# Optimization experiments

Measured on AMD Instinct MI355X. Metric: run time of the kernel, lower is better.

Reference implementation:

```python
import jax, jax.numpy as jnp
import numpy as np

NOISE_STD = 0.1

def setup_inputs() -> dict:
    key = jax.random.key(0)
    k1, k2, k3, k4 = jax.random.split(key, 4)
    B, S, D, E, NS = 4, 4096, 2048, 64, 10
    x = jax.random.normal(k1, (B, S, D), dtype=jnp.float32)
    W = jax.random.normal(k2, (E, D), dtype=jnp.float32) * (1.0 / np.sqrt(D))
    scale_condition = jax.random.normal(k3, (NS, 1, 1), dtype=jnp.float32)
    noise = jax.random.normal(k4, (B, S, E), dtype=jnp.float32)
    return {"x": x, "W": W, "scale_condition": scale_condition, "noise": noise, "scale_idx": 3}

def reference(x, W, scale_condition, noise, scale_idx):
    TOP_K = 2
    E = W.shape[0]
    # scale modulation: scale_condition[scale_idx] has shape [1,1], broadcasts over [B,S,D]
    scale_factor = scale_condition[scale_idx]
    router_input = x * (1.0 + scale_factor * 0.1)
    # small GEMM: [B,S,D] x [D,E] -> [B,S,E]
    router_logits = jnp.einsum('bsd,ed->bse', router_input, W)
    router_logits = router_logits + noise * NOISE_STD
    routing_probs = jax.nn.softmax(router_logits, axis=-1)
    routing_weights, selected_experts = jax.lax.top_k(routing_probs, TOP_K)
    routing_weights = routing_weights / jnp.sum(routing_weights, axis=-1, keepdims=True)
    # scatter top-k normalized weights into dense [B,S,E] dispatch tensor
    dispatch_tensor = jnp.sum(
        jax.nn.one_hot(selected_experts, E, dtype=routing_weights.dtype)
        * routing_weights[..., None],
        axis=-2,
    )
    return dispatch_tensor, routing_probs, selected_experts
```

## Files before the change

### kernel.cpp

```cpp
#include <hip/hip_runtime.h>
#include <math.h>

#define D        2048
#define E        64
#define NROWS    16384

#define ROWS_PB  32
#define BKC      64
#define NCH      (D / BKC)
#define LDX      72
#define LDW      72
#define BUF_SHORTS 13824
#define WCVT_BYTES ((size_t)2 * E * D * sizeof(unsigned short))

#define LSCALE   2048.0f
#define S1       4.8828125e-4f
#define S2       2.384185791015625e-7f

typedef __attribute__((ext_vector_type(8))) _Float16 f16x8;
typedef __attribute__((ext_vector_type(4))) float f32x4;

__device__ __forceinline__ unsigned short f2h(float f) {
    union { _Float16 h; unsigned short u; } c;
    c.h = (_Float16)f;
    return c.u;
}
__device__ __forceinline__ float h2f(unsigned short u) {
    union { _Float16 h; unsigned short u; } c;
    c.u = u;
    return (float)c.h;
}

__global__ __launch_bounds__(256)
void w_cvt(const float* __restrict__ W,
           unsigned short* __restrict__ whi,
           unsigned short* __restrict__ wlo)
{
    const int i = (blockIdx.x * 256 + threadIdx.x) << 3;
    const float4 a = *(const float4*)(W + i);
    const float4 b = *(const float4*)(W + i + 4);
    float vv[8] = {a.x, a.y, a.z, a.w, b.x, b.y, b.z, b.w};
    unsigned int hw[4], lw[4];
#pragma unroll
    for (int j = 0; j < 4; ++j) {
        const unsigned short h0 = f2h(vv[2*j]);
        const unsigned short h1 = f2h(vv[2*j+1]);
        const unsigned short l0 = f2h((vv[2*j]   - h2f(h0)) * LSCALE);
        const unsigned short l1 = f2h((vv[2*j+1] - h2f(h1)) * LSCALE);
        hw[j] = (unsigned int)h0 | ((unsigned int)h1 << 16);
        lw[j] = (unsigned int)l0 | ((unsigned int)l1 << 16);
    }
    *(uint4*)(whi + i) = make_uint4(hw[0], hw[1], hw[2], hw[3]);
    *(uint4*)(wlo + i) = make_uint4(lw[0], lw[1], lw[2], lw[3]);
}

__global__ __launch_bounds__(256)
void moe_fused(const float* __restrict__ x,
               const unsigned short* __restrict__ whi,
               const unsigned short* __restrict__ wlo,
               const float* __restrict__ scond,
               const int* __restrict__ sidx,
               const float* __restrict__ noise,
               float* __restrict__ dispatch,
               float* __restrict__ probs,
               float* __restrict__ sel)
{
    __shared__ unsigned short smem[2 * BUF_SHORTS];

    const int t = threadIdx.x;
    const int l = t & 63;
    const int w = t >> 6;

    const float factor = 1.0f + 0.1f * scond[sidx[0]];

    const int xrow = t >> 3;
    const int xoct = t & 7;
    const int we_  = t >> 2;
    const int wko  = (t & 3) << 4;

    const int R  = (w >> 1) << 4;
    const int CB = (w & 1) << 5;
    const int fr = l & 15;
    const int fq = l >> 4;

    const int rowG0 = blockIdx.x * ROWS_PB;

    const float* xg = x + (size_t)(rowG0 + xrow) * D + (xoct << 3);
    const unsigned short* wgh = whi + (size_t)we_ * D + wko;
    const unsigned short* wgl = wlo + (size_t)we_ * D + wko;

    f32x4 acc0h = {0.f,0.f,0.f,0.f}, acc0m = {0.f,0.f,0.f,0.f}, acc0l = {0.f,0.f,0.f,0.f};
    f32x4 acc1h = {0.f,0.f,0.f,0.f}, acc1m = {0.f,0.f,0.f,0.f}, acc1l = {0.f,0.f,0.f,0.f};

    float4 xa = *(const float4*)(xg);
    float4 xb = *(const float4*)(xg + 4);
    uint4  wa = *(const uint4*)(wgh);
    uint4  wb = *(const uint4*)(wgh + 8);
    uint4  wc = *(const uint4*)(wgl);
    uint4  wd = *(const uint4*)(wgl + 8);

    for (int c = 0; c < NCH; ++c) {
        unsigned short* base = smem + (c & 1) * BUF_SHORTS;
        unsigned short* xh = base;
        unsigned short* xl = base + 2304;
        unsigned short* wh = base + 4608;
        unsigned short* wl = base + 9216;

        {
            float vv[8] = {xa.x * factor, xa.y * factor, xa.z * factor, xa.w * factor,
                           xb.x * factor, xb.y * factor, xb.z * factor, xb.w * factor};
            unsigned int xhw[4], xlw[4];
#pragma unroll
            for (int j = 0; j < 4; ++j) {
                const unsigned short h0 = f2h(vv[2*j]);
                const unsigned short h1 = f2h(vv[2*j+1]);
                const unsigned short l0 = f2h((vv[2*j]   - h2f(h0)) * LSCALE);
                const unsigned short l1 = f2h((vv[2*j+1] - h2f(h1)) * LSCALE);
                xhw[j] = (unsigned int)h0 | ((unsigned int)h1 << 16);
                xlw[j] = (unsigned int)l0 | ((unsigned int)l1 << 16);
            }
            const int o = xrow * LDX + (xoct << 3);
            *(uint4*)&xh[o] = make_uint4(xhw[0], xhw[1], xhw[2], xhw[3]);
            *(uint4*)&xl[o] = make_uint4(xlw[0], xlw[1], xlw[2], xlw[3]);
        }
        {
            const int o = we_ * LDW + wko;
            *(uint4*)&wh[o]     = wa;
            *(uint4*)&wh[o + 8] = wb;
            *(uint4*)&wl[o]     = wc;
            *(uint4*)&wl[o + 8] = wd;
        }

        __syncthreads();

        if (c + 1 < NCH) {
            const int k0 = (c + 1) << 6;
            xa = *(const float4*)(xg + k0);
            xb = *(const float4*)(xg + k0 + 4);
            wa = *(const uint4*)(wgh + k0);
            wb = *(const uint4*)(wgh + k0 + 8);
            wc = *(const uint4*)(wgl + k0);
            wd = *(const uint4*)(wgl + k0 + 8);
        }

#pragma unroll
        for (int ks = 0; ks < 2; ++ks) {
            const int ko = (ks << 5) + (fq << 3);
            const f16x8 ah  = *(const f16x8*)&xh[(R + fr) * LDX + ko];
            const f16x8 al  = *(const f16x8*)&xl[(R + fr) * LDX + ko];
            const f16x8 b0h = *(const f16x8*)&wh[(CB + fr) * LDW + ko];
            const f16x8 b0l = *(const f16x8*)&wl[(CB + fr) * LDW + ko];
            const f16x8 b1h = *(const f16x8*)&wh[(CB + 16 + fr) * LDW + ko];
            const f16x8 b1l = *(const f16x8*)&wl[(CB + 16 + fr) * LDW + ko];
            acc0h = __builtin_amdgcn_mfma_f32_16x16x32_f16(ah, b0h, acc0h, 0, 0, 0);
            acc0m = __builtin_amdgcn_mfma_f32_16x16x32_f16(ah, b0l, acc0m, 0, 0, 0);
            acc0m = __builtin_amdgcn_mfma_f32_16x16x32_f16(al, b0h, acc0m, 0, 0, 0);
            acc0l = __builtin_amdgcn_mfma_f32_16x16x32_f16(al, b0l, acc0l, 0, 0, 0);
            acc1h = __builtin_amdgcn_mfma_f32_16x16x32_f16(ah, b1h, acc1h, 0, 0, 0);
            acc1m = __builtin_amdgcn_mfma_f32_16x16x32_f16(ah, b1l, acc1m, 0, 0, 0);
            acc1m = __builtin_amdgcn_mfma_f32_16x16x32_f16(al, b1h, acc1m, 0, 0, 0);
            acc1l = __builtin_amdgcn_mfma_f32_16x16x32_f16(al, b1l, acc1l, 0, 0, 0);
        }
    }

    __syncthreads();
    float* lg = (float*)smem;
#pragma unroll
    for (int j = 0; j < 4; ++j) {
        const int rr = R + (fq << 2) + j;
        lg[rr * 68 + CB + fr]      = acc0h[j] + S1 * acc0m[j] + S2 * acc0l[j];
        lg[rr * 68 + CB + 16 + fr] = acc1h[j] + S1 * acc1m[j] + S2 * acc1l[j];
    }
    __syncthreads();

    const int r0 = w << 3;
    float nz[8];
#pragma unroll
    for (int i = 0; i < 8; ++i)
        nz[i] = noise[(size_t)(rowG0 + r0 + i) * E + l];

#pragma unroll 2
    for (int i = 0; i < 8; ++i) {
        const int G = rowG0 + r0 + i;
        const float v = lg[(r0 + i) * 68 + l] + 0.1f * nz[i];

        float m = v;
#pragma unroll
        for (int off = 32; off > 0; off >>= 1)
            m = fmaxf(m, __shfl_xor(m, off, 64));
        const float p = expf(v - m);
        float s = p;
#pragma unroll
        for (int off = 32; off > 0; off >>= 1)
            s += __shfl_xor(s, off, 64);
        const float prob = p / s;
        probs[(size_t)G * E + l] = prob;

        float bv = prob; int bi = l;
#pragma unroll
        for (int off = 32; off > 0; off >>= 1) {
            const float ov = __shfl_xor(bv, off, 64);
            const int   oi = __shfl_xor(bi, off, 64);
            if (ov > bv || (ov == bv && oi < bi)) { bv = ov; bi = oi; }
        }
        float cv = (l == bi) ? -INFINITY : prob;
        int ci = l;
#pragma unroll
        for (int off = 32; off > 0; off >>= 1) {
            const float ov = __shfl_xor(cv, off, 64);
            const int   oi = __shfl_xor(ci, off, 64);
            if (ov > cv || (ov == cv && oi < ci)) { cv = ov; ci = oi; }
        }

        const float sum2 = bv + cv;
        float dval = 0.f;
        if (l == bi) dval = bv / sum2;
        if (l == ci) dval = cv / sum2;
        dispatch[(size_t)G * E + l] = dval;

        if (l == 0) {
            float2 sv; sv.x = (float)bi; sv.y = (float)ci;
            *(float2*)(sel + (size_t)G * 2) = sv;
        }
    }
}

__global__ __launch_bounds__(256)
void gemm_r2(const float* __restrict__ x, const float* __restrict__ W,
             const float* __restrict__ scond, const float* __restrict__ noise,
             const int* __restrict__ sidx, float* __restrict__ logits_out)
{
    __shared__ float4 xsb[32][17];
    __shared__ float4 wsh[64][16];
    const int tid = threadIdx.x;
    const int rowBase = blockIdx.x * 32;
    const float factor = 1.0f + 0.1f * scond[sidx[0]];
    const int xk = tid & 15, xr = tid >> 4, we = tid & 63, wk = tid >> 6;
    const int eg = tid & 15, rg = tid >> 4, e0 = eg << 2;
    float acc[2][4];
#pragma unroll
    for (int i = 0; i < 2; ++i)
#pragma unroll
        for (int j = 0; j < 4; ++j) acc[i][j] = 0.f;
    const float* xg = x + (size_t)rowBase * D;
    float4 xb[2], wb[4];
#pragma unroll
    for (int i = 0; i < 2; ++i)
        xb[i] = *(const float4*)(xg + (xr + 16 * i) * D + (xk << 2));
#pragma unroll
    for (int j = 0; j < 4; ++j)
        wb[j] = *(const float4*)(W + we * D + (wk << 4) + (j << 2));
    for (int t = 0; t < 32; ++t) {
#pragma unroll
        for (int i = 0; i < 2; ++i) {
            float4 v = xb[i];
            v.x *= factor; v.y *= factor; v.z *= factor; v.w *= factor;
            xsb[xr + 16 * i][xk] = v;
        }
        float* wsf = (float*)wsh;
#pragma unroll
        for (int j = 0; j < 4; ++j) {
            const int kk = (wk << 4) + (j << 2);
            wsf[(kk + 0) * E + we] = wb[j].x;
            wsf[(kk + 1) * E + we] = wb[j].y;
            wsf[(kk + 2) * E + we] = wb[j].z;
            wsf[(kk + 3) * E + we] = wb[j].w;
        }
        __syncthreads();
        if (t + 1 < 32) {
            const int k0 = (t + 1) * 64;
#pragma unroll
            for (int i = 0; i < 2; ++i)
                xb[i] = *(const float4*)(xg + (xr + 16 * i) * D + k0 + (xk << 2));
#pragma unroll
            for (int j = 0; j < 4; ++j)
                wb[j] = *(const float4*)(W + we * D + k0 + (wk << 4) + (j << 2));
        }
#pragma unroll
        for (int kg = 0; kg < 16; ++kg) {
            float4 xv[2], wv[4];
#pragma unroll
            for (int i = 0; i < 2; ++i) xv[i] = xsb[rg + 16 * i][kg];
#pragma unroll
            for (int c = 0; c < 4; ++c) wv[c] = wsh[(kg << 2) + c][eg];
#pragma unroll
            for (int i = 0; i < 2; ++i) {
                const float x0 = xv[i].x, x1 = xv[i].y, x2 = xv[i].z, x3 = xv[i].w;
                acc[i][0] += x0 * wv[0].x; acc[i][1] += x0 * wv[0].y;
                acc[i][2] += x0 * wv[0].z; acc[i][3] += x0 * wv[0].w;
                acc[i][0] += x1 * wv[1].x; acc[i][1] += x1 * wv[1].y;
                acc[i][2] += x1 * wv[1].z; acc[i][3] += x1 * wv[1].w;
                acc[i][0] += x2 * wv[2].x; acc[i][1] += x2 * wv[2].y;
                acc[i][2] += x2 * wv[2].z; acc[i][3] += x2 * wv[2].w;
                acc[i][0] += x3 * wv[3].x; acc[i][1] += x3 * wv[3].y;
                acc[i][2] += x3 * wv[3].z; acc[i][3] += x3 * wv[3].w;
            }
        }
        __syncthreads();
    }
#pragma unroll
    for (int i = 0; i < 2; ++i) {
        const int gRow = rowBase + rg + 16 * i;
        const float4 nz = *(const float4*)(noise + (size_t)gRow * E + e0);
        float4 o;
        o.x = acc[i][0] + 0.1f * nz.x; o.y = acc[i][1] + 0.1f * nz.y;
        o.z = acc[i][2] + 0.1f * nz.z; o.w = acc[i][3] + 0.1f * nz.w;
        *(float4*)(logits_out + (size_t)gRow * E + e0) = o;
    }
}

__global__ __launch_bounds__(256)
void topk_r2(float* __restrict__ probs, float* __restrict__ dispatch,
             float* __restrict__ sel)
{
    const int lane = threadIdx.x & 63;
    const int wave = threadIdx.x >> 6;
    const int row  = blockIdx.x * 4 + wave;
    const float v = probs[(size_t)row * E + lane];
    float m = v;
#pragma unroll
    for (int off = 32; off > 0; off >>= 1)
        m = fmaxf(m, __shfl_xor(m, off, 64));
    const float p = expf(v - m);
    float s = p;
#pragma unroll
    for (int off = 32; off > 0; off >>= 1)
        s += __shfl_xor(s, off, 64);
    const float prob = p / s;
    probs[(size_t)row * E + lane] = prob;
    float bv = prob; int bi = lane;
#pragma unroll
    for (int off = 32; off > 0; off >>= 1) {
        const float ov = __shfl_xor(bv, off, 64);
        const int   oi = __shfl_xor(bi, off, 64);
        if (ov > bv || (ov == bv && oi < bi)) { bv = ov; bi = oi; }
    }
    float cv = (lane == bi) ? -INFINITY : prob;
    int ci = lane;
#pragma unroll
    for (int off = 32; off > 0; off >>= 1) {
        const float ov = __shfl_xor(cv, off, 64);
        const int   oi = __shfl_xor(ci, off, 64);
        if (ov > cv || (ov == cv && oi < ci)) { cv = ov; ci = oi; }
    }
    const float sum2 = bv + cv;
    float dval = 0.f;
    if (lane == bi) dval = bv / sum2;
    if (lane == ci) dval = cv / sum2;
    dispatch[(size_t)row * E + lane] = dval;
    if (lane == 0) {
        float2 sv; sv.x = (float)bi; sv.y = (float)ci;
        *(float2*)(sel + (size_t)row * 2) = sv;
    }
}

extern "C" void kernel_launch(void* const* d_in, const int* in_sizes, int n_in,
                              void* d_out, int out_size, void* d_ws, size_t ws_size,
                              hipStream_t stream) {
    const float* x     = (const float*)d_in[0];
    const float* W     = (const float*)d_in[1];
    const float* scond = (const float*)d_in[2];
    const float* noise = (const float*)d_in[3];
    const int*   sidx  = (const int*)d_in[4];

    float* out      = (float*)d_out;
    float* dispatch = out;
    float* probs    = out + (size_t)NROWS * E;
    float* sel      = out + 2 * (size_t)NROWS * E;

    if (ws_size >= WCVT_BYTES) {
        unsigned short* whi = (unsigned short*)d_ws;
        unsigned short* wlo = whi + (size_t)E * D;
        w_cvt<<<dim3(64), dim3(256), 0, stream>>>(W, whi, wlo);
        moe_fused<<<dim3(NROWS / ROWS_PB), dim3(256), 0, stream>>>(
            x, whi, wlo, scond, sidx, noise, dispatch, probs, sel);
    } else {
        gemm_r2<<<dim3(NROWS / 32), dim3(256), 0, stream>>>(
            x, W, scond, noise, sidx, probs);
        topk_r2<<<dim3(NROWS / 4), dim3(256), 0, stream>>>(
            probs, dispatch, sel);
    }
}
```

Baseline: 223.7 us.

## Shrink row tile to 16 and stream W fragments directly into registers

Halves rows per block to 16, giving twice as many blocks, and gives each wave its own 16-expert column slice. W hi/lo fragments are now loaded straight from global memory into MFMA operand registers instead of being staged through shared memory. The X tile is prefetched two chunks ahead, and the LDS footprint drops to the X buffers only. The aim is higher occupancy and less LDS traffic and sync cost. In exchange, W is reread from global/L2 by every block, which doubles total W traffic.

```diff
diff --git a/kernel.cpp b/kernel.cpp
--- a/kernel.cpp
+++ b/kernel.cpp
@@ -5,12 +5,12 @@
 #define E        64
 #define NROWS    16384
 
-#define ROWS_PB  32
+#define ROWS_PB  16
 #define BKC      64
 #define NCH      (D / BKC)
 #define LDX      72
-#define LDW      72
-#define BUF_SHORTS 13824
+#define XBUF     (ROWS_PB * LDX)
+#define BUF_SHORTS (2 * XBUF)
 #define WCVT_BYTES ((size_t)2 * E * D * sizeof(unsigned short))
 
 #define LSCALE   2048.0f
@@ -73,93 +73,82 @@
 
     const float factor = 1.0f + 0.1f * scond[sidx[0]];
 
-    const int xrow = t >> 3;
-    const int xoct = t & 7;
-    const int we_  = t >> 2;
-    const int wko  = (t & 3) << 4;
-
-    const int R  = (w >> 1) << 4;
-    const int CB = (w & 1) << 5;
+    const int srow = t >> 4;
+    const int scol = (t & 15) << 2;
+
+    const int CB = w << 4;
     const int fr = l & 15;
     const int fq = l >> 4;
 
     const int rowG0 = blockIdx.x * ROWS_PB;
 
-    const float* xg = x + (size_t)(rowG0 + xrow) * D + (xoct << 3);
-    const unsigned short* wgh = whi + (size_t)we_ * D + wko;
-    const unsigned short* wgl = wlo + (size_t)we_ * D + wko;
-
-    f32x4 acc0h = {0.f,0.f,0.f,0.f}, acc0m = {0.f,0.f,0.f,0.f}, acc0l = {0.f,0.f,0.f,0.f};
-    f32x4 acc1h = {0.f,0.f,0.f,0.f}, acc1m = {0.f,0.f,0.f,0.f}, acc1l = {0.f,0.f,0.f,0.f};
-
-    float4 xa = *(const float4*)(xg);
-    float4 xb = *(const float4*)(xg + 4);
-    uint4  wa = *(const uint4*)(wgh);
-    uint4  wb = *(const uint4*)(wgh + 8);
-    uint4  wc = *(const uint4*)(wgl);
-    uint4  wd = *(const uint4*)(wgl + 8);
+    const float* xg = x + (size_t)(rowG0 + srow) * D + scol;
+    const unsigned short* wgh = whi + (size_t)(CB + fr) * D + (fq << 3);
+    const unsigned short* wgl = wlo + (size_t)(CB + fr) * D + (fq << 3);
+
+    f32x4 acch = {0.f,0.f,0.f,0.f};
+    f32x4 accm = {0.f,0.f,0.f,0.f};
+    f32x4 accl = {0.f,0.f,0.f,0.f};
+
+    float4 xf0 = *(const float4*)(xg);
+    float4 xf1 = *(const float4*)(xg + BKC);
+    f16x8 pbh0 = *(const f16x8*)(wgh);
+    f16x8 pbh1 = *(const f16x8*)(wgh + 32);
+    f16x8 pbl0 = *(const f16x8*)(wgl);
+    f16x8 pbl1 = *(const f16x8*)(wgl + 32);
 
     for (int c = 0; c < NCH; ++c) {
-        unsigned short* base = smem + (c & 1) * BUF_SHORTS;
-        unsigned short* xh = base;
-        unsigned short* xl = base + 2304;
-        unsigned short* wh = base + 4608;
-        unsigned short* wl = base + 9216;
+        unsigned short* xh = smem + (c & 1) * BUF_SHORTS;
+        unsigned short* xl = xh + XBUF;
 
         {
-            float vv[8] = {xa.x * factor, xa.y * factor, xa.z * factor, xa.w * factor,
-                           xb.x * factor, xb.y * factor, xb.z * factor, xb.w * factor};
-            unsigned int xhw[4], xlw[4];
-#pragma unroll
-            for (int j = 0; j < 4; ++j) {
-                const unsigned short h0 = f2h(vv[2*j]);
-                const unsigned short h1 = f2h(vv[2*j+1]);
-                const unsigned short l0 = f2h((vv[2*j]   - h2f(h0)) * LSCALE);
-                const unsigned short l1 = f2h((vv[2*j+1] - h2f(h1)) * LSCALE);
-                xhw[j] = (unsigned int)h0 | ((unsigned int)h1 << 16);
-                xlw[j] = (unsigned int)l0 | ((unsigned int)l1 << 16);
-            }
-            const int o = xrow * LDX + (xoct << 3);
-            *(uint4*)&xh[o] = make_uint4(xhw[0], xhw[1], xhw[2], xhw[3]);
-            *(uint4*)&xl[o] = make_uint4(xlw[0], xlw[1], xlw[2], xlw[3]);
-        }
+            const float v0 = xf0.x * factor, v1 = xf0.y * factor;
+            const float v2 = xf0.z * factor, v3 = xf0.w * factor;
+            const unsigned short h0 = f2h(v0), h1 = f2h(v1);
+            const unsigned short h2 = f2h(v2), h3 = f2h(v3);
+            const unsigned short q0 = f2h((v0 - h2f(h0)) * LSCALE);
+            const unsigned short q1 = f2h((v1 - h2f(h1)) * LSCALE);
+            const unsigned short q2 = f2h((v2 - h2f(h2)) * LSCALE);
+            const unsigned short q3 = f2h((v3 - h2f(h3)) * LSCALE);
+            uint2 hw, lw;
+            hw.x = (unsigned int)h0 | ((unsigned int)h1 << 16);
+            hw.y = (unsigned int)h2 | ((unsigned int)h3 << 16);
+            lw.x = (unsigned int)q0 | ((unsigned int)q1 << 16);
+            lw.y = (unsigned int)q2 | ((unsigned int)q3 << 16);
+            const int o = srow * LDX + scol;
+            *(uint2*)&xh[o] = hw;
+            *(uint2*)&xl[o] = lw;
+        }
+
+        __syncthreads();
+
+        xf0 = xf1;
+        if (c + 2 < NCH)
+            xf1 = *(const float4*)(xg + (c + 2) * BKC);
+
+        const f16x8 bh0 = pbh0, bh1 = pbh1, bl0 = pbl0, bl1 = pbl1;
+        if (c + 1 < NCH) {
+            const int kn = (c + 1) << 6;
+            pbh0 = *(const f16x8*)(wgh + kn);
+            pbh1 = *(const f16x8*)(wgh + kn + 32);
+            pbl0 = *(const f16x8*)(wgl + kn);
+            pbl1 = *(const f16x8*)(wgl + kn + 32);
+        }
+
         {
-            const int o = we_ * LDW + wko;
-            *(uint4*)&wh[o]     = wa;
-            *(uint4*)&wh[o + 8] = wb;
-            *(uint4*)&wl[o]     = wc;
-            *(uint4*)&wl[o + 8] = wd;
-        }
-
-        __syncthreads();
-
-        if (c + 1 < NCH) {
-            const int k0 = (c + 1) << 6;
-            xa = *(const float4*)(xg + k0);
-            xb = *(const float4*)(xg + k0 + 4);
-            wa = *(const uint4*)(wgh + k0);
-            wb = *(const uint4*)(wgh + k0 + 8);
-            wc = *(const uint4*)(wgl + k0);
-            wd = *(const uint4*)(wgl + k0 + 8);
-        }
-
-#pragma unroll
-        for (int ks = 0; ks < 2; ++ks) {
-            const int ko = (ks << 5) + (fq << 3);
-            const f16x8 ah  = *(const f16x8*)&xh[(R + fr) * LDX + ko];
-            const f16x8 al  = *(const f16x8*)&xl[(R + fr) * LDX + ko];
-            const f16x8 b0h = *(const f16x8*)&wh[(CB + fr) * LDW + ko];
-            const f16x8 b0l = *(const f16x8*)&wl[(CB + fr) * LDW + ko];
-            const f16x8 b1h = *(const f16x8*)&wh[(CB + 16 + fr) * LDW + ko];
-            const f16x8 b1l = *(const f16x8*)&wl[(CB + 16 + fr) * LDW + ko];
-            acc0h = __builtin_amdgcn_mfma_f32_16x16x32_f16(ah, b0h, acc0h, 0, 0, 0);
-            acc0m = __builtin_amdgcn_mfma_f32_16x16x32_f16(ah, b0l, acc0m, 0, 0, 0);
-            acc0m = __builtin_amdgcn_mfma_f32_16x16x32_f16(al, b0h, acc0m, 0, 0, 0);
-            acc0l = __builtin_amdgcn_mfma_f32_16x16x32_f16(al, b0l, acc0l, 0, 0, 0);
-            acc1h = __builtin_amdgcn_mfma_f32_16x16x32_f16(ah, b1h, acc1h, 0, 0, 0);
-            acc1m = __builtin_amdgcn_mfma_f32_16x16x32_f16(ah, b1l, acc1m, 0, 0, 0);
-            acc1m = __builtin_amdgcn_mfma_f32_16x16x32_f16(al, b1h, acc1m, 0, 0, 0);
-            acc1l = __builtin_amdgcn_mfma_f32_16x16x32_f16(al, b1l, acc1l, 0, 0, 0);
+            const int ko = fq << 3;
+            const f16x8 ah0 = *(const f16x8*)&xh[fr * LDX + ko];
+            const f16x8 al0 = *(const f16x8*)&xl[fr * LDX + ko];
+            const f16x8 ah1 = *(const f16x8*)&xh[fr * LDX + 32 + ko];
+            const f16x8 al1 = *(const f16x8*)&xl[fr * LDX + 32 + ko];
+            acch = __builtin_amdgcn_mfma_f32_16x16x32_f16(ah0, bh0, acch, 0, 0, 0);
+            accm = __builtin_amdgcn_mfma_f32_16x16x32_f16(ah0, bl0, accm, 0, 0, 0);
+            accm = __builtin_amdgcn_mfma_f32_16x16x32_f16(al0, bh0, accm, 0, 0, 0);
+            accl = __builtin_amdgcn_mfma_f32_16x16x32_f16(al0, bl0, accl, 0, 0, 0);
+            acch = __builtin_amdgcn_mfma_f32_16x16x32_f16(ah1, bh1, acch, 0, 0, 0);
+            accm = __builtin_amdgcn_mfma_f32_16x16x32_f16(ah1, bl1, accm, 0, 0, 0);
+            accm = __builtin_amdgcn_mfma_f32_16x16x32_f16(al1, bh1, accm, 0, 0, 0);
+            accl = __builtin_amdgcn_mfma_f32_16x16x32_f16(al1, bl1, accl, 0, 0, 0);
         }
     }
 
@@ -167,22 +156,16 @@
     float* lg = (float*)smem;
 #pragma unroll
     for (int j = 0; j < 4; ++j) {
-        const int rr = R + (fq << 2) + j;
-        lg[rr * 68 + CB + fr]      = acc0h[j] + S1 * acc0m[j] + S2 * acc0l[j];
-        lg[rr * 68 + CB + 16 + fr] = acc1h[j] + S1 * acc1m[j] + S2 * acc1l[j];
+        const int rr = (fq << 2) + j;
+        lg[rr * 68 + CB + fr] = acch[j] + S1 * accm[j] + S2 * accl[j];
     }
     __syncthreads();
 
-    const int r0 = w << 3;
-    float nz[8];
-#pragma unroll
-    for (int i = 0; i < 8; ++i)
-        nz[i] = noise[(size_t)(rowG0 + r0 + i) * E + l];
-
-#pragma unroll 2
-    for (int i = 0; i < 8; ++i) {
+    const int r0 = w << 2;
+#pragma unroll
+    for (int i = 0; i < 4; ++i) {
         const int G = rowG0 + r0 + i;
-        const float v = lg[(r0 + i) * 68 + l] + 0.1f * nz[i];
+        const float v = lg[(r0 + i) * 68 + l] + 0.1f * noise[(size_t)G * E + l];
 
         float m = v;
 #pragma unroll
```

Result: slower. 241.0 us (+7.7%).
